# Performance work log

Measured on AMD Instinct MI355X. Metric: run time of the kernel, lower is better.

## Reference

```python
import jax, jax.numpy as jnp
import numpy as np

HEADS = 8
DK = 64            # key_size == size_per_head
NEIGHBORS = 3
KSIZE = 1 + 2 * NEIGHBORS  # 7 (rate=1)


def setup_inputs() -> dict:
    key = jax.random.key(0)
    k1, k2, k3, k4 = jax.random.split(key, 4)
    B, HW, S, D = 2, 64, 256, 512
    inputs = jax.random.normal(k1, (B, HW, S, D), dtype=jnp.float32)
    pos_bias = jax.random.normal(k2, (HEADS, S, KSIZE), dtype=jnp.float32)
    W_qkv = jax.random.normal(k3, (D, 3 * HEADS * DK), dtype=jnp.float32) * 0.02
    W_out = jax.random.normal(k4, (HEADS * DK, D), dtype=jnp.float32) * 0.02
    return {"inputs": inputs, "pos_bias": pos_bias, "W_qkv": W_qkv, "W_out": W_out}


def reference(inputs, pos_bias, W_qkv, W_out):
    B, HW, S, D = inputs.shape
    # qkv projection (no bias), split into q, k, v
    qkv = inputs @ W_qkv                                   # [B,HW,S,3*H*DK]
    q, k, v = jnp.split(qkv, 3, axis=-1)
    q = (q / jnp.sqrt(jnp.float32(DK))).reshape(B, HW, S, HEADS, DK)
    k = k.reshape(B, HW, S, HEADS, DK)
    v = v.reshape(B, HW, S, HEADS, DK)

    # zero-pad keys/values along seq (faithful to F.pad with value=0)
    pad = NEIGHBORS
    kp = jnp.pad(k, ((0, 0), (0, 0), (pad, pad), (0, 0), (0, 0)))
    vp = jnp.pad(v, ((0, 0), (0, 0), (pad, pad), (0, 0), (0, 0)))

    # sliding-window gather: window w for query i covers padded positions i..i+KSIZE-1
    idx = jnp.arange(S)[:, None] + jnp.arange(KSIZE)[None, :]  # [S,KSIZE]
    kw = kp[:, :, idx]                                         # [B,HW,S,KSIZE,H,DK]
    vw = vp[:, :, idx]                                         # [B,HW,S,KSIZE,H,DK]

    # scores over the window
    attn = jnp.einsum('bnshd,bnswhd->bnswh', q, kw)            # [B,HW,S,KSIZE,H]
    # additive positional bias: [H,S,KSIZE] -> [S,KSIZE,H] broadcast
    attn = attn + jnp.transpose(pos_bias, (1, 2, 0))[None, None]
    attn = jax.nn.softmax(attn, axis=-2)                       # softmax over window dim

    out = jnp.einsum('bnswh,bnswhd->bnshd', attn, vw)          # [B,HW,S,H,DK]
    out = out.reshape(B, HW, S, HEADS * DK)
    return out @ W_out
```

## Files before the change

kernel.cpp:

```cpp
#include <hip/hip_runtime.h>
#include <hip/hip_bf16.h>
#include <cstdint>


typedef __bf16 bf16x8 __attribute__((ext_vector_type(8)));
typedef float f32x4 __attribute__((ext_vector_type(4)));

__device__ __forceinline__ uint16_t f2bf(float f) {
    uint32_t u = __builtin_bit_cast(uint32_t, f);
    return (uint16_t)((u + 0x7fffu + ((u >> 16) & 1u)) >> 16);
}
__device__ __forceinline__ float bflo(uint32_t u) { return __builtin_bit_cast(float, u << 16); }
__device__ __forceinline__ float bfhi(uint32_t u) { return __builtin_bit_cast(float, u & 0xffff0000u); }

__device__ __forceinline__ void unpack8(uint4 v, float* f) {
    f[0] = bflo(v.x); f[1] = bfhi(v.x);
    f[2] = bflo(v.y); f[3] = bfhi(v.y);
    f[4] = bflo(v.z); f[5] = bfhi(v.z);
    f[6] = bflo(v.w); f[7] = bfhi(v.w);
}
__device__ __forceinline__ uint32_t pack2(float a, float b) {
    return (uint32_t)f2bf(a) | ((uint32_t)f2bf(b) << 16);
}

#define GLOAD_LDS16(gp, lp)                                                        \
    __builtin_amdgcn_global_load_lds((const __attribute__((address_space(1))) void*)(gp), \
                                     (__attribute__((address_space(3))) void*)(lp), 16, 0, 0)

__device__ __forceinline__ bf16x8 ds_read16(const uint16_t* p) {
    bf16x8 r;
    asm volatile("ds_read_b128 %0, %1"
                 : "=v"(r)
                 : "v"((const __attribute__((address_space(3))) void*)p));
    return r;
}

__device__ __forceinline__ uint4 gload16(const uint16_t* p) {
    uint4 r;
    asm volatile("global_load_dwordx4 %0, %1, off"
                 : "=v"(r)
                 : "v"((const __attribute__((address_space(1))) void*)p));
    return r;
}

__global__ void cvt_f32_bf16(const float* __restrict__ in, uint16_t* __restrict__ out, int n8) {
    int i = blockIdx.x * 256 + threadIdx.x;
    if (i >= n8) return;
    const float4* p = (const float4*)in + (size_t)i * 2;
    float4 a = p[0], b = p[1];
    uint4 o;
    o.x = pack2(a.x, a.y);
    o.y = pack2(a.z, a.w);
    o.z = pack2(b.x, b.y);
    o.w = pack2(b.z, b.w);
    *((uint4*)out + i) = o;
}

__global__ void transpose_cvt(const float* __restrict__ in, uint16_t* __restrict__ out,
                              int R, int C) {
    int idx = blockIdx.x * 256 + threadIdx.x;
    if (idx >= R * C) return;
    int r = idx / C;
    int c = idx - r * C;
    out[(size_t)c * R + r] = f2bf(in[idx]);
}

template <bool F32OUT>
__global__ __launch_bounds__(512, 4)
void gemm_mn(const uint16_t* __restrict__ A, const uint16_t* __restrict__ BT,
             void* __restrict__ Cout, int M, int N, int K) {
    __shared__ __align__(16) uint16_t lds[36864];

    const int tid  = threadIdx.x;
    const int lane = tid & 63;
    const int wv   = tid >> 6;
    const int r    = lane & 15;
    const int quad = lane >> 4;
    const int wr   = wv >> 1;
    const int wc   = wv & 1;
    const long bm0 = (long)blockIdx.x * 256;
    const long bn0 = (long)blockIdx.y * 128;
    const int NT   = K >> 5;

#define SRC_ROWCOL(d_, row_, col_) do {                                                 \
        int ln_ = (d_) >> 3, pre_ = ((d_) & 7) ^ (ln_ & 7);                             \
        row_ = 2 * ln_ + (pre_ >> 2);                                                   \
        col_ = (pre_ & 3) * 8;                                                          \
    } while (0)
    int rA0, cA0, rA1, cA1, rB0, cB0;
    SRC_ROWCOL(tid,       rA0, cA0);
    SRC_ROWCOL(tid + 512, rA1, cA1);
    SRC_ROWCOL(tid,       rB0, cB0);
    const uint16_t* pA0 = A  + (bm0 + rA0) * (long)K + cA0;
    const uint16_t* pA1 = A  + (bm0 + rA1) * (long)K + cA1;
    const uint16_t* pB0 = BT + (bn0 + rB0) * (long)K + cB0;
#undef SRC_ROWCOL

#define STAGE(b_, t_) do {                                                              \
        GLOAD_LDS16(pA0 + (t_) * 32, &lds[(b_) * 8192 + tid * 8]);                      \
        GLOAD_LDS16(pA1 + (t_) * 32, &lds[(b_) * 8192 + (tid + 512) * 8]);              \
        GLOAD_LDS16(pB0 + (t_) * 32, &lds[24576 + (b_) * 4096 + tid * 8]);              \
    } while (0)

    const int p_ln  = (((r & 1) << 2) | quad) ^ ((r >> 1) & 7);
    const int aLane = wr * 2048 + (r >> 1) * 64 + p_ln * 8;
    const int bLane = 24576 + wc * 2048 + (r >> 1) * 64 + p_ln * 8;

#define DS_A(mf_) ds_read16(&lds[aoff + aLane + (mf_) * 512])
#define DS_B(nf_) ds_read16(&lds[boff + bLane + (nf_) * 512])

#define WAITK2 do { asm volatile("s_waitcnt lgkmcnt(2)" ::: "memory");                  \
                    __builtin_amdgcn_sched_barrier(0); } while (0)
#define WAITK0 do { asm volatile("s_waitcnt lgkmcnt(0)" ::: "memory");                  \
                    __builtin_amdgcn_sched_barrier(0); } while (0)

#define MFMA_CL(m0_, f0_, f1_)                                                          \
    __builtin_amdgcn_s_setprio(1);                                                      \
    _Pragma("unroll")                                                                   \
    for (int nf = 0; nf < 4; ++nf)                                                      \
        acc[(m0_)][nf] = __builtin_amdgcn_mfma_f32_16x16x32_bf16(f0_, bfr[nf],          \
                                                                 acc[(m0_)][nf], 0, 0, 0); \
    _Pragma("unroll")                                                                   \
    for (int nf = 0; nf < 4; ++nf)                                                      \
        acc[(m0_) + 1][nf] = __builtin_amdgcn_mfma_f32_16x16x32_bf16(f1_, bfr[nf],      \
                                                                 acc[(m0_) + 1][nf], 0, 0, 0); \
    __builtin_amdgcn_s_setprio(0);

    f32x4 acc[4][4];
#pragma unroll
    for (int mf = 0; mf < 4; ++mf)
#pragma unroll
        for (int nf = 0; nf < 4; ++nf) acc[mf][nf] = (f32x4){0.f, 0.f, 0.f, 0.f};

    STAGE(0, 0);
    STAGE(1, 1);
    asm volatile("s_waitcnt vmcnt(3)" ::: "memory");
    __builtin_amdgcn_s_barrier();

    int b = 0, bs = 2;
    for (int t = 0; t < NT; ++t) {
        const int aoff = b * 8192;
        const int boff = b * 4096;

        if (t + 2 < NT) STAGE(bs, t + 2);

        bf16x8 bfr[4], a0, a1, a2, a3;
#pragma unroll
        for (int nf = 0; nf < 4; ++nf) bfr[nf] = DS_B(nf);
        a0 = DS_A(0); a1 = DS_A(1);
        a2 = DS_A(2); a3 = DS_A(3);

        WAITK2;
        MFMA_CL(0, a0, a1)

        WAITK0;
        MFMA_CL(2, a2, a3)

        if (t + 1 < NT) {
            if (t + 2 < NT)
                asm volatile("s_waitcnt vmcnt(3)" ::: "memory");
            else
                asm volatile("s_waitcnt vmcnt(0)" ::: "memory");
            __builtin_amdgcn_s_barrier();
        }

        b  = (b  == 2) ? 0 : b + 1;
        bs = (bs == 2) ? 0 : bs + 1;
    }

#pragma unroll
    for (int mf = 0; mf < 4; ++mf) {
#pragma unroll
        for (int i = 0; i < 4; ++i) {
            long m = bm0 + wr * 64 + mf * 16 + quad * 4 + i;
            if (F32OUT) {
                float* crow = (float*)Cout + m * (long)N + bn0 + wc * 64 + r;
#pragma unroll
                for (int nf = 0; nf < 4; ++nf) crow[nf * 16] = acc[mf][nf][i];
            } else {
                uint16_t* crow = (uint16_t*)Cout + m * (long)N + bn0 + wc * 64 + r;
#pragma unroll
                for (int nf = 0; nf < 4; ++nf) crow[nf * 16] = f2bf(acc[mf][nf][i]);
            }
        }
    }
#undef STAGE
#undef DS_A
#undef DS_B
#undef WAITK2
#undef WAITK0
#undef MFMA_CL
}

__global__ __launch_bounds__(256, 2)
void local_attn(const uint16_t* __restrict__ qkv, const float* __restrict__ pb,
                uint16_t* __restrict__ attn) {
    __shared__ __align__(16) uint4 smem[4192];

    const int h  = blockIdx.x & 7;
    const int bn = blockIdx.x >> 3;
    const int s  = threadIdx.x;
    const int tid = threadIdx.x;
    const size_t base = (size_t)bn * 256 * 1536;

    const uint16_t* qrow = qkv + base + (size_t)s * 1536 + h * 64;
    uint4 qc[8];
#pragma unroll
    for (int c = 0; c < 8; ++c) qc[c] = gload16(qrow + c * 8);

    if (tid < 96) {
        int a    = tid / 48;
        int rem  = tid - a * 48;
        int hr6  = rem >> 3;
        int c8   = rem & 7;
        int hrow = (hr6 < 3) ? hr6 : (256 + hr6);
        smem[a * 2096 + hrow * 8 + c8] = (uint4){0u, 0u, 0u, 0u};
    }

#pragma unroll
    for (int it = 0; it < 16; ++it) {
        int i   = tid + it * 256;
        int a   = i >> 11;
        int idx = i & 2047;
        int sp  = idx >> 3;
        int cs  = (i & 7) ^ ((sp + 3) & 7);
        const uint16_t* src = qkv + base + (size_t)sp * 1536 + 512 + a * 512 + h * 64 + cs * 8;
        GLOAD_LDS16(src, (uint16_t*)&smem[a * 2096 + (sp + 3) * 8 + (i & 7)]);
    }

    asm volatile("s_waitcnt vmcnt(8) lgkmcnt(0)" ::: "memory");
    __builtin_amdgcn_s_barrier();
    __builtin_amdgcn_sched_barrier(0);

    float sc[7];
#pragma unroll
    for (int w = 0; w < 7; ++w) sc[w] = 0.f;

#pragma unroll
    for (int c = 0; c < 8; ++c) {
        float qf[8];
        unpack8(qc[c], qf);
        uint4 kc[7];
#pragma unroll
        for (int w = 0; w < 7; ++w) {
            int hrow = s + w;
            kc[w] = smem[hrow * 8 + (c ^ (hrow & 7))];
        }
#pragma unroll
        for (int w = 0; w < 7; ++w) {
            float kf[8];
            unpack8(kc[w], kf);
#pragma unroll
            for (int j = 0; j < 8; ++j) sc[w] += qf[j] * kf[j];
        }
    }

    const float* pbr = pb + ((size_t)h * 256 + s) * 7;
    float mx = -1e30f;
#pragma unroll
    for (int w = 0; w < 7; ++w) {
        sc[w] = sc[w] * 0.125f + pbr[w];
        mx = fmaxf(mx, sc[w]);
    }
    float p[7], sum = 0.f;
#pragma unroll
    for (int w = 0; w < 7; ++w) {
        p[w] = __expf(sc[w] - mx);
        sum += p[w];
    }
    const float inv = 1.f / sum;
#pragma unroll
    for (int w = 0; w < 7; ++w) p[w] *= inv;

    asm volatile("s_waitcnt vmcnt(0)" ::: "memory");
    __builtin_amdgcn_s_barrier();
    __builtin_amdgcn_sched_barrier(0);

    uint4 ov[8];
#pragma unroll
    for (int c = 0; c < 8; ++c) {
        uint4 vc[7];
#pragma unroll
        for (int w = 0; w < 7; ++w) {
            int hrow = s + w;
            vc[w] = smem[2096 + hrow * 8 + (c ^ (hrow & 7))];
        }
        float o[8] = {0.f, 0.f, 0.f, 0.f, 0.f, 0.f, 0.f, 0.f};
#pragma unroll
        for (int w = 0; w < 7; ++w) {
            float vf[8];
            unpack8(vc[w], vf);
#pragma unroll
            for (int j = 0; j < 8; ++j) o[j] += p[w] * vf[j];
        }
        ov[c].x = pack2(o[0], o[1]);
        ov[c].y = pack2(o[2], o[3]);
        ov[c].z = pack2(o[4], o[5]);
        ov[c].w = pack2(o[6], o[7]);
    }

    uint16_t* orow = attn + ((size_t)(bn * 256 + s)) * 512 + h * 64;
#pragma unroll
    for (int c = 0; c < 8; ++c) *(uint4*)(orow + c * 8) = ov[c];
}

extern "C" void kernel_launch(void* const* d_in, const int* in_sizes, int n_in,
                              void* d_out, int out_size, void* d_ws, size_t ws_size,
                              hipStream_t stream) {
    const float* X    = (const float*)d_in[0];
    const float* pb   = (const float*)d_in[1];
    const float* Wqkv = (const float*)d_in[2];
    const float* Wout = (const float*)d_in[3];
    float* out = (float*)d_out;

    char* ws = (char*)d_ws;
    uint16_t* WqkvT = (uint16_t*)(ws);
    uint16_t* WoutT = (uint16_t*)(ws + 1572864);
    uint16_t* qkvb  = (uint16_t*)(ws + 2097152);
    uint16_t* Xb    = (uint16_t*)(ws + 102760448);
    uint16_t* attnb = Xb;

    cvt_f32_bf16<<<(32768 * 512 / 8 + 255) / 256, 256, 0, stream>>>(X, Xb, 32768 * 512 / 8);
    transpose_cvt<<<(512 * 1536 + 255) / 256, 256, 0, stream>>>(Wqkv, WqkvT, 512, 1536);
    transpose_cvt<<<(512 * 512 + 255) / 256, 256, 0, stream>>>(Wout, WoutT, 512, 512);

    gemm_mn<false><<<dim3(128, 12), 512, 0, stream>>>(Xb, WqkvT, qkvb, 32768, 1536, 512);
    local_attn<<<1024, 256, 0, stream>>>(qkvb, pb, attnb);
    gemm_mn<true><<<dim3(128, 4), 512, 0, stream>>>(attnb, WoutT, out, 32768, 512, 512);
}
```

Baseline: 257.1 us.

## Fuse QKV projection GEMM with local window attention per head tile

Replaces the separate QKV GEMM and local attention kernels with one kernel. Each block computes Q/K/V for one head over 256 rows, writes them into LDS and runs the 7-wide windowed softmax attention there, so the large bf16 qkv intermediate never goes to global memory. The two weight transpose kernels are also merged into one launch. The fused GEMM uses a 256x192 tile with double buffering instead of triple, at lower occupancy and with a heavier LDS footprint.

```diff
diff --git a/kernel.cpp b/kernel.cpp
--- a/kernel.cpp
+++ b/kernel.cpp
@@ -32,14 +32,6 @@
     asm volatile("ds_read_b128 %0, %1"
                  : "=v"(r)
                  : "v"((const __attribute__((address_space(3))) void*)p));
-    return r;
-}
-
-__device__ __forceinline__ uint4 gload16(const uint16_t* p) {
-    uint4 r;
-    asm volatile("global_load_dwordx4 %0, %1, off"
-                 : "=v"(r)
-                 : "v"((const __attribute__((address_space(1))) void*)p));
     return r;
 }
 
@@ -56,13 +48,241 @@
     *((uint4*)out + i) = o;
 }
 
-__global__ void transpose_cvt(const float* __restrict__ in, uint16_t* __restrict__ out,
-                              int R, int C) {
+__global__ void transpose_cvt2(const float* __restrict__ Wqkv, const float* __restrict__ Wout,
+                               uint16_t* __restrict__ WqkvT, uint16_t* __restrict__ WoutT) {
     int idx = blockIdx.x * 256 + threadIdx.x;
-    if (idx >= R * C) return;
-    int r = idx / C;
-    int c = idx - r * C;
-    out[(size_t)c * R + r] = f2bf(in[idx]);
+    if (idx < 512 * 1536) {
+        int r = idx / 1536, c = idx - r * 1536;
+        WqkvT[(size_t)c * 512 + r] = f2bf(Wqkv[idx]);
+    } else {
+        idx -= 512 * 1536;
+        int r = idx >> 9, c = idx & 511;
+        WoutT[(size_t)c * 512 + r] = f2bf(Wout[idx]);
+    }
+}
+
+__global__ __launch_bounds__(512, 2)
+void gemm_qkv_attn(const uint16_t* __restrict__ Xb, const uint16_t* __restrict__ WqkvT,
+                   const float* __restrict__ pb, uint16_t* __restrict__ attn) {
+    __shared__ __align__(16) uint16_t lds[54016];
+
+    constexpr int KO = 16384;
+    constexpr int VO = 33152;
+    constexpr int PO = 49920;
+
+    const int tid  = threadIdx.x;
+    const int lane = tid & 63;
+    const int wv   = tid >> 6;
+    const int r    = lane & 15;
+    const int quad = lane >> 4;
+    const int wr   = wv >> 1;
+    const int wc   = wv & 1;
+    const int h    = blockIdx.x >> 7;
+    const int bn   = blockIdx.x & 127;
+    const long bm0 = (long)bn * 256;
+    const int NT   = 16;
+
+#define SRC_ROWCOL(d_, row_, col_) do {                                                 \
+        int ln_ = (d_) >> 3, pre_ = ((d_) & 7) ^ (ln_ & 7);                             \
+        row_ = 2 * ln_ + (pre_ >> 2);                                                   \
+        col_ = (pre_ & 3) * 8;                                                          \
+    } while (0)
+    int rA0, cA0, rA1, cA1, rB0, cB0, rB1, cB1;
+    SRC_ROWCOL(tid,        rA0, cA0);
+    SRC_ROWCOL(tid + 512,  rA1, cA1);
+    SRC_ROWCOL(tid,        rB0, cB0);
+    SRC_ROWCOL(tid + 512,  rB1, cB1);
+#undef SRC_ROWCOL
+    const long gB0 = ((long)(rB0 >> 6)) * 512 + h * 64 + (rB0 & 63);
+    const long gB1 = ((long)(rB1 >> 6)) * 512 + h * 64 + (rB1 & 63);
+    const uint16_t* pA0 = Xb + (bm0 + rA0) * 512L + cA0;
+    const uint16_t* pA1 = Xb + (bm0 + rA1) * 512L + cA1;
+    const uint16_t* pB0 = WqkvT + gB0 * 512 + cB0;
+    const uint16_t* pB1 = WqkvT + gB1 * 512 + cB1;
+
+#define STAGE(b_, t_) do {                                                              \
+        GLOAD_LDS16(pA0 + (t_) * 32, &lds[(b_) * 8192 + tid * 8]);                      \
+        GLOAD_LDS16(pA1 + (t_) * 32, &lds[(b_) * 8192 + (tid + 512) * 8]);              \
+        GLOAD_LDS16(pB0 + (t_) * 32, &lds[16384 + (b_) * 6144 + tid * 8]);              \
+        if (tid < 256)                                                                  \
+            GLOAD_LDS16(pB1 + (t_) * 32, &lds[16384 + (b_) * 6144 + (tid + 512) * 8]);  \
+    } while (0)
+
+    const int p_ln  = (((r & 1) << 2) | quad) ^ ((r >> 1) & 7);
+    const int aLane = wr * 2048 + (r >> 1) * 64 + p_ln * 8;
+    const int bLane = 16384 + wc * 3072 + (r >> 1) * 64 + p_ln * 8;
+
+#define DS_A(mf_) ds_read16(&lds[aoff + aLane + (mf_) * 512])
+#define DS_B(nf_) ds_read16(&lds[boff + bLane + (nf_) * 512])
+#define WAITK(n_) do { asm volatile("s_waitcnt lgkmcnt(" #n_ ")" ::: "memory");         \
+                       __builtin_amdgcn_sched_barrier(0); } while (0)
+
+    f32x4 acc[4][6];
+#pragma unroll
+    for (int mf = 0; mf < 4; ++mf)
+#pragma unroll
+        for (int nf = 0; nf < 6; ++nf) acc[mf][nf] = (f32x4){0.f, 0.f, 0.f, 0.f};
+
+    STAGE(0, 0);
+    asm volatile("s_waitcnt vmcnt(0)" ::: "memory");
+    __builtin_amdgcn_s_barrier();
+
+    for (int t = 0; t < NT; ++t) {
+        const int b    = t & 1;
+        const int aoff = b * 8192;
+        const int boff = b * 6144;
+        const bool pf  = (t + 1 < NT);
+
+        if (pf) STAGE(b ^ 1, t + 1);
+
+        bf16x8 bfr[6], a0, a1, a2, a3;
+#pragma unroll
+        for (int nf = 0; nf < 6; ++nf) bfr[nf] = DS_B(nf);
+        a0 = DS_A(0); a1 = DS_A(1);
+        a2 = DS_A(2); a3 = DS_A(3);
+
+        WAITK(2);
+        __builtin_amdgcn_s_setprio(1);
+#pragma unroll
+        for (int nf = 0; nf < 6; ++nf) {
+            acc[0][nf] = __builtin_amdgcn_mfma_f32_16x16x32_bf16(a0, bfr[nf], acc[0][nf], 0, 0, 0);
+            acc[1][nf] = __builtin_amdgcn_mfma_f32_16x16x32_bf16(a1, bfr[nf], acc[1][nf], 0, 0, 0);
+        }
+        __builtin_amdgcn_s_setprio(0);
+
+        WAITK(0);
+        __builtin_amdgcn_s_setprio(1);
+#pragma unroll
+        for (int nf = 0; nf < 6; ++nf) {
+            acc[2][nf] = __builtin_amdgcn_mfma_f32_16x16x32_bf16(a2, bfr[nf], acc[2][nf], 0, 0, 0);
+            acc[3][nf] = __builtin_amdgcn_mfma_f32_16x16x32_bf16(a3, bfr[nf], acc[3][nf], 0, 0, 0);
+        }
+        __builtin_amdgcn_s_setprio(0);
+
+        if (pf) {
+            asm volatile("s_waitcnt vmcnt(0)" ::: "memory");
+            __builtin_amdgcn_s_barrier();
+        }
+    }
+
+    asm volatile("s_waitcnt vmcnt(0) lgkmcnt(0)" ::: "memory");
+    __builtin_amdgcn_s_barrier();
+
+    if (tid < 96) {
+        int a    = tid / 48;
+        int rem  = tid - a * 48;
+        int hr6  = rem >> 3;
+        int c8   = rem & 7;
+        int hrow = (hr6 < 3) ? hr6 : (256 + hr6);
+        ((uint4*)&lds[a ? VO : KO])[hrow * 8 + c8] = (uint4){0u, 0u, 0u, 0u};
+    }
+
+#pragma unroll
+    for (int nf = 0; nf < 6; ++nf) {
+        int arr, d0;
+        if (wc == 0) { if (nf < 4) { arr = 0; d0 = nf * 16; } else { arr = 1; d0 = (nf - 4) * 16; } }
+        else         { if (nf < 2) { arr = 1; d0 = 32 + nf * 16; } else { arr = 2; d0 = (nf - 2) * 16; } }
+        const int d    = d0 + r;
+        const int base = (arr == 0) ? 0 : ((arr == 1) ? KO : VO);
+        const int hofs = (arr == 0) ? 0 : 3;
+#pragma unroll
+        for (int mf = 0; mf < 4; ++mf) {
+#pragma unroll
+            for (int i = 0; i < 4; ++i) {
+                int row  = wr * 64 + mf * 16 + quad * 4 + i;
+                int rowX = row + hofs;
+                int off  = base + rowX * 64 + ((((d >> 3) ^ (rowX & 7))) << 3) + (d & 7);
+                lds[off] = f2bf(acc[mf][nf][i]);
+            }
+        }
+    }
+    __syncthreads();
+
+    const int s     = tid & 255;
+    const int half  = tid >> 8;
+    const int cbase = half * 4;
+    float* pp = (float*)&lds[PO];
+
+    uint4 qc[4];
+    const uint4* qarr = (const uint4*)lds;
+#pragma unroll
+    for (int c = 0; c < 4; ++c) qc[c] = qarr[s * 8 + ((cbase + c) ^ (s & 7))];
+
+    float sc[7];
+#pragma unroll
+    for (int w = 0; w < 7; ++w) sc[w] = 0.f;
+    const uint4* karr = (const uint4*)&lds[KO];
+#pragma unroll
+    for (int c = 0; c < 4; ++c) {
+        float qf[8];
+        unpack8(qc[c], qf);
+#pragma unroll
+        for (int w = 0; w < 7; ++w) {
+            int hrow = s + w;
+            uint4 kc = karr[hrow * 8 + ((cbase + c) ^ (hrow & 7))];
+            float kf[8];
+            unpack8(kc, kf);
+#pragma unroll
+            for (int j = 0; j < 8; ++j) sc[w] += qf[j] * kf[j];
+        }
+    }
+
+    if (half == 1) {
+#pragma unroll
+        for (int w = 0; w < 7; ++w) pp[s * 8 + w] = sc[w];
+    }
+    __syncthreads();
+
+    if (half == 0) {
+        const float* pbr = pb + ((size_t)h * 256 + s) * 7;
+        float mx = -1e30f, tot[7];
+#pragma unroll
+        for (int w = 0; w < 7; ++w) {
+            tot[w] = (sc[w] + pp[s * 8 + w]) * 0.125f + pbr[w];
+            mx = fmaxf(mx, tot[w]);
+        }
+        float sum = 0.f;
+#pragma unroll
+        for (int w = 0; w < 7; ++w) {
+            tot[w] = __expf(tot[w] - mx);
+            sum += tot[w];
+        }
+        const float inv = 1.f / sum;
+#pragma unroll
+        for (int w = 0; w < 7; ++w) pp[s * 8 + w] = tot[w] * inv;
+    }
+    __syncthreads();
+
+    float p[7];
+#pragma unroll
+    for (int w = 0; w < 7; ++w) p[w] = pp[s * 8 + w];
+
+    const uint4* varr = (const uint4*)&lds[VO];
+    uint4 ov[4];
+#pragma unroll
+    for (int c = 0; c < 4; ++c) {
+        float o[8] = {0.f, 0.f, 0.f, 0.f, 0.f, 0.f, 0.f, 0.f};
+#pragma unroll
+        for (int w = 0; w < 7; ++w) {
+            int hrow = s + w;
+            uint4 vc = varr[hrow * 8 + ((cbase + c) ^ (hrow & 7))];
+            float vf[8];
+            unpack8(vc, vf);
+#pragma unroll
+            for (int j = 0; j < 8; ++j) o[j] += p[w] * vf[j];
+        }
+        ov[c].x = pack2(o[0], o[1]);
+        ov[c].y = pack2(o[2], o[3]);
+        ov[c].z = pack2(o[4], o[5]);
+        ov[c].w = pack2(o[6], o[7]);
+    }
+    uint16_t* orow = attn + ((size_t)(bn * 256 + s)) * 512 + h * 64 + cbase * 8;
+#pragma unroll
+    for (int c = 0; c < 4; ++c) *(uint4*)(orow + c * 8) = ov[c];
+#undef STAGE
+#undef DS_A
+#undef DS_B
+#undef WAITK
 }
 
 template <bool F32OUT>
@@ -108,12 +328,10 @@
 
 #define DS_A(mf_) ds_read16(&lds[aoff + aLane + (mf_) * 512])
 #define DS_B(nf_) ds_read16(&lds[boff + bLane + (nf_) * 512])
-
 #define WAITK2 do { asm volatile("s_waitcnt lgkmcnt(2)" ::: "memory");                  \
                     __builtin_amdgcn_sched_barrier(0); } while (0)
 #define WAITK0 do { asm volatile("s_waitcnt lgkmcnt(0)" ::: "memory");                  \
                     __builtin_amdgcn_sched_barrier(0); } while (0)
-
 #define MFMA_CL(m0_, f0_, f1_)                                                          \
     __builtin_amdgcn_s_setprio(1);                                                      \
     _Pragma("unroll")                                                                   \
@@ -152,7 +370,6 @@
 
         WAITK2;
         MFMA_CL(0, a0, a1)
-
         WAITK0;
         MFMA_CL(2, a2, a3)
 
@@ -163,7 +380,6 @@
                 asm volatile("s_waitcnt vmcnt(0)" ::: "memory");
             __builtin_amdgcn_s_barrier();
         }
-
         b  = (b  == 2) ? 0 : b + 1;
         bs = (bs == 2) ? 0 : bs + 1;
     }
@@ -190,118 +406,6 @@
 #undef WAITK2
 #undef WAITK0
 #undef MFMA_CL
-}
-
-__global__ __launch_bounds__(256, 2)
-void local_attn(const uint16_t* __restrict__ qkv, const float* __restrict__ pb,
-                uint16_t* __restrict__ attn) {
-    __shared__ __align__(16) uint4 smem[4192];
-
-    const int h  = blockIdx.x & 7;
-    const int bn = blockIdx.x >> 3;
-    const int s  = threadIdx.x;
-    const int tid = threadIdx.x;
-    const size_t base = (size_t)bn * 256 * 1536;
-
-    const uint16_t* qrow = qkv + base + (size_t)s * 1536 + h * 64;
-    uint4 qc[8];
-#pragma unroll
-    for (int c = 0; c < 8; ++c) qc[c] = gload16(qrow + c * 8);
-
-    if (tid < 96) {
-        int a    = tid / 48;
-        int rem  = tid - a * 48;
-        int hr6  = rem >> 3;
-        int c8   = rem & 7;
-        int hrow = (hr6 < 3) ? hr6 : (256 + hr6);
-        smem[a * 2096 + hrow * 8 + c8] = (uint4){0u, 0u, 0u, 0u};
-    }
-
-#pragma unroll
-    for (int it = 0; it < 16; ++it) {
-        int i   = tid + it * 256;
-        int a   = i >> 11;
-        int idx = i & 2047;
-        int sp  = idx >> 3;
-        int cs  = (i & 7) ^ ((sp + 3) & 7);
-        const uint16_t* src = qkv + base + (size_t)sp * 1536 + 512 + a * 512 + h * 64 + cs * 8;
-        GLOAD_LDS16(src, (uint16_t*)&smem[a * 2096 + (sp + 3) * 8 + (i & 7)]);
-    }
-
-    asm volatile("s_waitcnt vmcnt(8) lgkmcnt(0)" ::: "memory");
-    __builtin_amdgcn_s_barrier();
-    __builtin_amdgcn_sched_barrier(0);
-
-    float sc[7];
-#pragma unroll
-    for (int w = 0; w < 7; ++w) sc[w] = 0.f;
-
-#pragma unroll
-    for (int c = 0; c < 8; ++c) {
-        float qf[8];
-        unpack8(qc[c], qf);
-        uint4 kc[7];
-#pragma unroll
-        for (int w = 0; w < 7; ++w) {
-            int hrow = s + w;
-            kc[w] = smem[hrow * 8 + (c ^ (hrow & 7))];
-        }
-#pragma unroll
-        for (int w = 0; w < 7; ++w) {
-            float kf[8];
-            unpack8(kc[w], kf);
-#pragma unroll
-            for (int j = 0; j < 8; ++j) sc[w] += qf[j] * kf[j];
-        }
-    }
-
-    const float* pbr = pb + ((size_t)h * 256 + s) * 7;
-    float mx = -1e30f;
-#pragma unroll
-    for (int w = 0; w < 7; ++w) {
-        sc[w] = sc[w] * 0.125f + pbr[w];
-        mx = fmaxf(mx, sc[w]);
-    }
-    float p[7], sum = 0.f;
-#pragma unroll
-    for (int w = 0; w < 7; ++w) {
-        p[w] = __expf(sc[w] - mx);
-        sum += p[w];
-    }
-    const float inv = 1.f / sum;
-#pragma unroll
-    for (int w = 0; w < 7; ++w) p[w] *= inv;
-
-    asm volatile("s_waitcnt vmcnt(0)" ::: "memory");
-    __builtin_amdgcn_s_barrier();
-    __builtin_amdgcn_sched_barrier(0);
-
-    uint4 ov[8];
-#pragma unroll
-    for (int c = 0; c < 8; ++c) {
-        uint4 vc[7];
-#pragma unroll
-        for (int w = 0; w < 7; ++w) {
-            int hrow = s + w;
-            vc[w] = smem[2096 + hrow * 8 + (c ^ (hrow & 7))];
-        }
-        float o[8] = {0.f, 0.f, 0.f, 0.f, 0.f, 0.f, 0.f, 0.f};
-#pragma unroll
-        for (int w = 0; w < 7; ++w) {
-            float vf[8];
-            unpack8(vc[w], vf);
-#pragma unroll
-            for (int j = 0; j < 8; ++j) o[j] += p[w] * vf[j];
-        }
-        ov[c].x = pack2(o[0], o[1]);
-        ov[c].y = pack2(o[2], o[3]);
-        ov[c].z = pack2(o[4], o[5]);
-        ov[c].w = pack2(o[6], o[7]);
-    }
-
-    uint16_t* orow = attn + ((size_t)(bn * 256 + s)) * 512 + h * 64;
-#pragma unroll
-    for (int c = 0; c < 8; ++c) *(uint4*)(orow + c * 8) = ov[c];
 }
 
 extern "C" void kernel_launch(void* const* d_in, const int* in_sizes, int n_in,
@@ -316,15 +420,12 @@
     char* ws = (char*)d_ws;
     uint16_t* WqkvT = (uint16_t*)(ws);
     uint16_t* WoutT = (uint16_t*)(ws + 1572864);
-    uint16_t* qkvb  = (uint16_t*)(ws + 2097152);
-    uint16_t* Xb    = (uint16_t*)(ws + 102760448);
-    uint16_t* attnb = Xb;
+    uint16_t* Xb    = (uint16_t*)(ws + 2097152);
+    uint16_t* attnb = (uint16_t*)(ws + 35651584);
 
     cvt_f32_bf16<<<(32768 * 512 / 8 + 255) / 256, 256, 0, stream>>>(X, Xb, 32768 * 512 / 8);
-    transpose_cvt<<<(512 * 1536 + 255) / 256, 256, 0, stream>>>(Wqkv, WqkvT, 512, 1536);
-    transpose_cvt<<<(512 * 512 + 255) / 256, 256, 0, stream>>>(Wout, WoutT, 512, 512);
-
-    gemm_mn<false><<<dim3(128, 12), 512, 0, stream>>>(Xb, WqkvT, qkvb, 32768, 1536, 512);
-    local_attn<<<1024, 256, 0, stream>>>(qkvb, pb, attnb);
+    transpose_cvt2<<<(512 * 2048 + 255) / 256, 256, 0, stream>>>(Wqkv, Wout, WqkvT, WoutT);
+
+    gemm_qkv_attn<<<1024, 512, 0, stream>>>(Xb, WqkvT, pb, attnb);
     gemm_mn<true><<<dim3(128, 4), 512, 0, stream>>>(attnb, WoutT, out, 32768, 512, 512);
 }
```

Result: faster. 236.6 us (-8.0%).
